# Optimization experiments

Hardware: AMD Instinct MI355X
Metric: run time of the kernel (lower is better)

The kernel has to match this reference:

```python
import jax, jax.numpy as jnp
import numpy as np

N0 = 100000; E0 = 1600000; N1 = 100000; E1 = 1600000; G = 512
F0 = 93; F1 = 43
BN_EPS = 1e-5


def setup_inputs() -> dict:
    key = jax.random.key(0)
    ks = jax.random.split(key, 20)
    p = lambda i, shape: jax.random.normal(ks[i], shape, jnp.float32) * 0.02
    return {
        "x_0": jax.random.normal(ks[0], (N0, F0), jnp.float32),
        "x_1": jax.random.normal(ks[1], (N1, F1), jnp.float32),
        "edge_index_0": jax.random.randint(ks[2], (2, E0), 0, N0, jnp.int32),
        "edge_index_1": jax.random.randint(ks[3], (2, E1), 0, N1, jnp.int32),
        "batch_0": jnp.sort(jax.random.randint(ks[4], (N0,), 0, G, jnp.int32)),
        "batch_1": jnp.sort(jax.random.randint(ks[5], (N1,), 0, G, jnp.int32)),
        "w_c1": p(6, (F0, F0)), "b_c1": jnp.zeros((F0,), jnp.float32),
        "w_c2": p(7, (F0, F0 * 10)), "b_c2": jnp.zeros((F0 * 10,), jnp.float32),
        "w_c3": p(8, (F1, F1)), "b_c3": jnp.zeros((F1,), jnp.float32),
        "w_c4": p(9, (F1, F1 * 10)), "b_c4": jnp.zeros((F1 * 10,), jnp.float32),
        "g0_w1": p(10, (F0 * 10 * 2, 1024)), "g0_b1": jnp.zeros((1024,), jnp.float32),
        "g0_w2": p(11, (1024, 512)), "g0_b2": jnp.zeros((512,), jnp.float32),
        "g0_bn_g": jnp.ones((512,), jnp.float32), "g0_bn_b": jnp.zeros((512,), jnp.float32),
        "g1_w1": p(12, (F1 * 10 * 2, 1024)), "g1_b1": jnp.zeros((1024,), jnp.float32),
        "g1_w2": p(13, (1024, 512)), "g1_b2": jnp.zeros((512,), jnp.float32),
        "g1_bn_g": jnp.ones((512,), jnp.float32), "g1_bn_b": jnp.zeros((512,), jnp.float32),
        "f0_w1": p(14, (512, 256)), "f0_b1": jnp.zeros((256,), jnp.float32),
        "f0_w2": p(15, (256, 2)), "f0_b2": jnp.zeros((2,), jnp.float32),
        "f1_w1": p(16, (512, 256)), "f1_b1": jnp.zeros((256,), jnp.float32),
        "f1_w2": p(17, (256, 2)), "f1_b2": jnp.zeros((2,), jnp.float32),
    }


def gin_conv(x, edge_index, W, b):
    # GINConv(eps=0): nn(x + sum_{j->i} x_j); messages from src=edge_index[0] to dst=edge_index[1]
    agg = jax.ops.segment_sum(x[edge_index[0]], edge_index[1], num_segments=x.shape[0])
    return (x + agg) @ W + b


def pool_mean_max(x, batch):
    cnt = jax.ops.segment_sum(jnp.ones((x.shape[0], 1), x.dtype), batch, num_segments=G)
    mean = jax.ops.segment_sum(x, batch, num_segments=G) / jnp.maximum(cnt, 1.0)
    mx = jax.ops.segment_max(x, batch, num_segments=G)
    mx = jnp.where(cnt > 0, mx, 0.0)
    return jnp.concatenate([mean, mx], axis=1)


def batchnorm(x, g, b):
    m = x.mean(axis=0)
    v = x.var(axis=0)
    return g * (x - m) / jnp.sqrt(v + BN_EPS) + b


def branch(x, ei, batch, w_a, b_a, w_b, b_b, w1, b1, w2, b2, bn_g, bn_b):
    h = jax.nn.relu(gin_conv(x, ei, w_a, b_a))
    h = jax.nn.relu(gin_conv(h, ei, w_b, b_b))
    h = pool_mean_max(h, batch)              # [G, 2*10*F] ; PairNorm(mode='None') is identity
    h = jax.nn.relu(h @ w1 + b1)             # dropout: eval mode (identity)
    h = h @ w2 + b2
    return batchnorm(h, bn_g, bn_b)          # [G, 512]


def reference(x_0, x_1, edge_index_0, edge_index_1, batch_0, batch_1,
              w_c1, b_c1, w_c2, b_c2, w_c3, b_c3, w_c4, b_c4,
              g0_w1, g0_b1, g0_w2, g0_b2, g0_bn_g, g0_bn_b,
              g1_w1, g1_b1, g1_w2, g1_b2, g1_bn_g, g1_bn_b,
              f0_w1, f0_b1, f0_w2, f0_b2, f1_w1, f1_b1, f1_w2, f1_b2):
    x_g_0 = branch(x_0, edge_index_0, batch_0, w_c1, b_c1, w_c2, b_c2,
                   g0_w1, g0_b1, g0_w2, g0_b2, g0_bn_g, g0_bn_b)
    z = jax.nn.relu(x_g_0 @ f0_w1 + f0_b1) @ f0_w2 + f0_b2
    x_g_1 = branch(x_1, edge_index_1, batch_1, w_c3, b_c3, w_c4, b_c4,
                   g1_w1, g1_b1, g1_w2, g1_b2, g1_bn_g, g1_bn_b)
    z1 = jax.nn.relu(x_g_1 @ f1_w1 + f1_b1) @ f1_w2 + f1_b2
    return (z, x_g_0, x_g_1, z1)
```

## Files before the change

### kernel.cpp

```cpp
#include <hip/hip_runtime.h>
#include <hip/hip_bf16.h>

#define N0 100000
#define E0C 1600000
#define N1 100000
#define E1C 1600000
#define GCONST 512
#define F0C 93
#define F1C 43
#define OC0 (F0C * 10)
#define OC1 (F1C * 10)
#define BN_EPS 1e-5f
#define NBKT 391
#define SLAB 6016

typedef __attribute__((ext_vector_type(8))) short short8;
typedef __attribute__((ext_vector_type(4))) float floatx4;

static __device__ __forceinline__ unsigned short f2bf(float f) {
    unsigned u = __float_as_uint(f);
    unsigned r = (u + 0x7FFF + ((u >> 16) & 1)) >> 16;
    return (unsigned short)r;
}
static __device__ __forceinline__ float bf2f(unsigned short u) {
    return __uint_as_float(((unsigned)u) << 16);
}
static __device__ __forceinline__ void split_bf(float v, unsigned short& h, unsigned short& l) {
    h = f2bf(v);
    l = f2bf(v - bf2f(h));
}

__global__ __launch_bounds__(256) void misc_kernel(const int* __restrict__ bat0,
                                                   const int* __restrict__ bat1,
                                                   int* __restrict__ st0,
                                                   int* __restrict__ st1,
                                                   int* __restrict__ bcur2,
                                                   float* __restrict__ bnsum0,
                                                   float* __restrict__ bnsum1) {
    int bid = blockIdx.x;
    int t = threadIdx.x;
    if (bid < 6) {
        int branch = bid / 3;
        const int* batch = branch ? bat1 : bat0;
        int* starts = branch ? st1 : st0;
        int g = (bid % 3) * 256 + t;
        if (g > GCONST) return;
        if (g == GCONST) { starts[GCONST] = N0; return; }
        int lo = 0, hi = N0;
        while (lo < hi) {
            int mid = (lo + hi) >> 1;
            if (batch[mid] < g) lo = mid + 1; else hi = mid;
        }
        starts[g] = lo;
    } else if (bid == 6) {
        for (int i = t; i < 1024; i += 256) {
            if (i < NBKT) bcur2[i] = i * SLAB;
            else if (i >= 512 && i < 512 + NBKT) bcur2[i] = (i - 512) * SLAB;
        }
    } else {
        for (int i = t; i < 1024; i += 256) {
            bnsum0[i] = 0.f;
            bnsum1[i] = 0.f;
        }
    }
}

__global__ __launch_bounds__(256) void edge_bucket2_kernel(const int* __restrict__ ei0,
                                                           const int* __restrict__ ei1,
                                                           int E, int* __restrict__ bcur2,
                                                           int2* __restrict__ st0,
                                                           int2* __restrict__ st1,
                                                           const float* __restrict__ Wc1,
                                                           const float* __restrict__ Wc2,
                                                           const float* __restrict__ Wc3,
                                                           const float* __restrict__ Wc4,
                                                           unsigned short* __restrict__ Ta0,
                                                           unsigned short* __restrict__ Tb0,
                                                           unsigned short* __restrict__ Ta1,
                                                           unsigned short* __restrict__ Tb1,
                                                           unsigned short* __restrict__ p0h,
                                                           unsigned short* __restrict__ p0l,
                                                           unsigned short* __restrict__ p1h,
                                                           unsigned short* __restrict__ p1l) {
    int bid = blockIdx.x;
    int t = threadIdx.x;
    if (bid < 1564) {
        int branch = bid >= 782;
        int blk = branch ? bid - 782 : bid;
        const int* ei = branch ? ei1 : ei0;
        int* bcur = bcur2 + branch * 512;
        int2* staging = branch ? st1 : st0;
        __shared__ int hist[NBKT];
        __shared__ int gbase[NBKT];
        for (int i = t; i < NBKT; i += 256) hist[i] = 0;
        __syncthreads();
        int base = blk * 2048;
        int srcv[8], dstv[8];
#pragma unroll
        for (int i = 0; i < 8; ++i) {
            int e = base + i * 256 + t;
            if (e < E) { srcv[i] = ei[e]; dstv[i] = ei[E + e]; }
            else dstv[i] = -1;
        }
#pragma unroll
        for (int i = 0; i < 8; ++i)
            if (dstv[i] >= 0) atomicAdd(&hist[dstv[i] >> 8], 1);
        __syncthreads();
        for (int i = t; i < NBKT; i += 256) {
            int c = hist[i];
            gbase[i] = c ? atomicAdd(&bcur[i], c) : 0;
            hist[i] = 0;
        }
        __syncthreads();
#pragma unroll
        for (int i = 0; i < 8; ++i) {
            if (dstv[i] >= 0) {
                int b = dstv[i] >> 8;
                int lofs = atomicAdd(&hist[b], 1);
                staging[gbase[b] + lofs] = make_int2(srcv[i], dstv[i]);
            }
        }
    } else if (bid < 3612) {
        int idx = bid - 1564;
        int cfg = idx >> 9;
        int c = (idx & 511) * 2 + (t >> 7);
        int k = t & 127;
        const float* W; unsigned short* T; int OCr, Fr, KP, RB;
        switch (cfg) {
            case 0:  W = Wc1; T = Ta0; OCr = 93;  Fr = 93; KP = 96; RB = 96;   break;
            case 1:  W = Wc2; T = Tb0; OCr = 930; Fr = 93; KP = 96; RB = 1024; break;
            case 2:  W = Wc3; T = Ta1; OCr = 43;  Fr = 43; KP = 64; RB = 48;   break;
            default: W = Wc4; T = Tb1; OCr = 430; Fr = 43; KP = 64; RB = 512;  break;
        }
        if (c >= RB || k >= KP) return;
        unsigned short v = 0;
        if (c < OCr && k < Fr) v = f2bf(W[(size_t)k * OCr + c]);
        T[(size_t)c * KP + k] = v;
    } else if (bid < 3732) {
        int i = (bid - 3612) * 256 + t;
        if (i >= GCONST * 60) return;
        int g = i / 60, c = 1860 + (i - g * 60);
        p0h[(size_t)g * 1920 + c] = 0;
        p0l[(size_t)g * 1920 + c] = 0;
    } else {
        int i = (bid - 3732) * 256 + t;
        if (i >= GCONST * 36) return;
        int g = i / 36, c = 860 + (i - g * 36);
        p1h[(size_t)g * 896 + c] = 0;
        p1l[(size_t)g * 896 + c] = 0;
    }
}

__global__ __launch_bounds__(512) void bucket_scan2_kernel(const int* __restrict__ bcur2,
                                                           int* __restrict__ bbase2) {
    const int* bcur = bcur2 + blockIdx.x * 512;
    int* bbase = bbase2 + blockIdx.x * 512;
    __shared__ int sh[512];
    int t = threadIdx.x;
    int cnt = (t < NBKT) ? bcur[t] - t * SLAB : 0;
    sh[t] = cnt;
    __syncthreads();
    for (int o = 1; o < 512; o <<= 1) {
        int add = (t >= o) ? sh[t - o] : 0;
        __syncthreads();
        sh[t] += add;
        __syncthreads();
    }
    if (t <= NBKT) bbase[t] = sh[t] - cnt;
}

static __device__ __forceinline__ void csr_build_dev(int b, const int2* __restrict__ staging,
                                                     const int* __restrict__ bcur,
                                                     const int* __restrict__ bbase, int N,
                                                     int* __restrict__ rowptr,
                                                     int* __restrict__ col) {
    __shared__ int h[256];
    __shared__ int sc[256];
    int t = threadIdx.x;
    int sl = b * SLAB;
    int se = bcur[b];
    int go = bbase[b];
    h[t] = 0;
    __syncthreads();
    for (int i = sl + t; i < se; i += 256)
        atomicAdd(&h[staging[i].y & 255], 1);
    __syncthreads();
    int v = h[t];
    sc[t] = v;
    __syncthreads();
    for (int o = 1; o < 256; o <<= 1) {
        int add = (t >= o) ? sc[t - o] : 0;
        __syncthreads();
        sc[t] += add;
        __syncthreads();
    }
    int ex = go + (sc[t] - v);
    int node = (b << 8) + t;
    if (node <= N) rowptr[node] = ex;
    __syncthreads();
    sc[t] = ex;
    __syncthreads();
    for (int i = sl + t; i < se; i += 256) {
        int2 ed = staging[i];
        int pos = atomicAdd(&sc[ed.y & 255], 1);
        col[pos] = ed.x;
    }
}

static __device__ __forceinline__ void wsplit_dev(int k0, int c0,
                                                  const float* __restrict__ W,
                                                  unsigned short* __restrict__ Th,
                                                  unsigned short* __restrict__ Tl,
                                                  int K, int N, int KP) {
    __shared__ float tile[32][33];
    int tx = threadIdx.x & 31, ty = threadIdx.x >> 5;
    for (int r = ty; r < 32; r += 8) {
        int k = k0 + r;
        tile[r][tx] = (k < K) ? W[(size_t)k * N + c0 + tx] : 0.f;
    }
    __syncthreads();
    for (int r = ty; r < 32; r += 8) {
        int c = c0 + r;
        float v = tile[tx][r];
        unsigned short h, l;
        split_bf(v, h, l);
        Th[(size_t)c * KP + k0 + tx] = h;
        Tl[(size_t)c * KP + k0 + tx] = l;
    }
}

template<int KP, int CH, int GR>
static __device__ __forceinline__ void gather_dev(int nb, unsigned short* __restrict__ t,
                                                  const unsigned short* __restrict__ x,
                                                  const int* __restrict__ rowptr,
                                                  const int* __restrict__ col, int N) {
    int wave = threadIdx.x >> 6, lane = threadIdx.x & 63;
    int node = nb * 4 + wave;
    if (node >= N) return;
    int g = lane / CH;
    int c = lane - g * CH;
    bool act = (g < GR);
    int s = rowptr[node], e = rowptr[node + 1];
    float acc[8] = {0.f, 0.f, 0.f, 0.f, 0.f, 0.f, 0.f, 0.f};
    int j = act ? (s - 1 + g) : e;
    int src0 = node;
    if (j >= s && j < e) src0 = col[j];
    while (j < e) {
        int jb = j + GR;
        int jc = jb + GR;
        int srcb = (jb < e) ? col[jb] : 0;
        int srcc = (jc < e) ? col[jc] : 0;
        short8 v0 = *(const short8*)(x + (size_t)src0 * KP + c * 8);
#pragma unroll
        for (int i = 0; i < 8; ++i) acc[i] += bf2f((unsigned short)v0[i]);
        if (jb < e) {
            short8 v1 = *(const short8*)(x + (size_t)srcb * KP + c * 8);
#pragma unroll
            for (int i = 0; i < 8; ++i) acc[i] += bf2f((unsigned short)v1[i]);
        }
        j = jc; src0 = srcc;
    }
    if (GR == 8) {
#pragma unroll
        for (int i = 0; i < 8; ++i) {
            float v = acc[i];
            v += __shfl_xor(v, 8);
            v += __shfl_xor(v, 16);
            v += __shfl_xor(v, 32);
            acc[i] = v;
        }
    } else {
#pragma unroll
        for (int i = 0; i < 8; ++i) {
            float v = acc[i];
            float v1 = __shfl(v, lane + CH);
            float v2 = __shfl(v, lane + 2 * CH);
            float v3 = __shfl(v, lane + 3 * CH);
            float v4 = __shfl(v, lane + 4 * CH);
            acc[i] = v + v1 + v2 + v3 + v4;
        }
    }
    if (lane < CH) {
        short8 o;
#pragma unroll
        for (int i = 0; i < 8; ++i) o[i] = (short)f2bf(acc[i]);
        *(short8*)(t + (size_t)node * KP + lane * 8) = o;
    }
}

template<int KP, int KS, int NT>
static __device__ __forceinline__ void conv1_dev(int nb, const unsigned short* __restrict__ t,
                                                 const unsigned short* __restrict__ Wt,
                                                 const float* __restrict__ bias,
                                                 unsigned short* __restrict__ y,
                                                 int NC, int N) {
    int wave = threadIdx.x >> 6, lane = threadIdx.x & 63;
    int quad = lane >> 4, l15 = lane & 15;
    int r0 = (nb * 4 + wave) * 16;
    const short8 z8 = {0, 0, 0, 0, 0, 0, 0, 0};
    short8 a[KS];
    int arow = r0 + l15;
#pragma unroll
    for (int ks = 0; ks < KS; ++ks)
        a[ks] = (arow < N) ? *(const short8*)(t + (size_t)arow * KP + ks * 32 + quad * 8) : z8;
#pragma unroll
    for (int nt = 0; nt < NT; ++nt) {
        int colb = nt * 16 + l15;
        floatx4 c = {0.f, 0.f, 0.f, 0.f};
#pragma unroll
        for (int ks = 0; ks < KS; ++ks) {
            short8 b = *(const short8*)(Wt + (size_t)colb * KP + ks * 32 + quad * 8);
            c = __builtin_amdgcn_mfma_f32_16x16x32_bf16(a[ks], b, c, 0, 0, 0);
        }
        float bc = (colb < NC) ? bias[colb] : 0.f;
#pragma unroll
        for (int r = 0; r < 4; ++r) {
            int row = r0 + quad * 4 + r;
            if (row < N) {
                float o = fmaxf(c[r] + bc, 0.f);
                y[(size_t)row * KP + colb] = f2bf(o);
            }
        }
    }
}

template<int KP, int KS>
static __device__ __forceinline__ void conv2_pool_dev(int cb, int g,
                                                      const unsigned short* __restrict__ t,
                                                      const unsigned short* __restrict__ Wt,
                                                      const float* __restrict__ bias,
                                                      const int* __restrict__ starts,
                                                      unsigned short* __restrict__ ph,
                                                      unsigned short* __restrict__ pl,
                                                      int OC, int KPad) {
    int wave = threadIdx.x >> 6, lane = threadIdx.x & 63;
    int quad = lane >> 4, l15 = lane & 15;
    int cw0 = cb * 256 + wave * 64;
    short8 bfr[4][KS];
    float bs[4];
#pragma unroll
    for (int ti = 0; ti < 4; ++ti) {
        int colb = cw0 + ti * 16 + l15;
#pragma unroll
        for (int ks = 0; ks < KS; ++ks)
            bfr[ti][ks] = *(const short8*)(Wt + (size_t)colb * KP + ks * 32 + quad * 8);
        bs[ti] = (colb < OC) ? bias[colb] : 0.f;
    }
    int s = starts[g], e = starts[g + 1];
    float sum[4] = {0.f, 0.f, 0.f, 0.f};
    float mx[4]  = {0.f, 0.f, 0.f, 0.f};
    const short8 z8 = {0, 0, 0, 0, 0, 0, 0, 0};
    for (int ns = s; ns < e; ns += 16) {
        short8 a[KS];
        int arow = ns + l15;
        bool av = arow < e;
#pragma unroll
        for (int ks = 0; ks < KS; ++ks)
            a[ks] = av ? *(const short8*)(t + (size_t)arow * KP + ks * 32 + quad * 8) : z8;
        int rbase = ns + quad * 4;
#pragma unroll
        for (int ti = 0; ti < 4; ++ti) {
            floatx4 c = {0.f, 0.f, 0.f, 0.f};
#pragma unroll
            for (int ks = 0; ks < KS; ++ks)
                c = __builtin_amdgcn_mfma_f32_16x16x32_bf16(a[ks], bfr[ti][ks], c, 0, 0, 0);
#pragma unroll
            for (int r = 0; r < 4; ++r) {
                float o = fmaxf(c[r] + bs[ti], 0.f);
                if (rbase + r < e) {
                    sum[ti] += o;
                    mx[ti] = fmaxf(mx[ti], o);
                }
            }
        }
    }
    int cnt = e - s;
    float rc = 1.f / (float)(cnt > 0 ? cnt : 1);
#pragma unroll
    for (int ti = 0; ti < 4; ++ti) {
        float sv = sum[ti], mv = mx[ti];
        sv += __shfl_down(sv, 32);
        mv = fmaxf(mv, __shfl_down(mv, 32));
        sv += __shfl_down(sv, 16);
        mv = fmaxf(mv, __shfl_down(mv, 16));
        if (lane < 16) {
            int colb = cw0 + ti * 16 + l15;
            if (colb < OC) {
                size_t base = (size_t)g * (size_t)KPad;
                unsigned short h, l;
                split_bf(sv * rc, h, l);
                ph[base + colb] = h; pl[base + colb] = l;
                split_bf(mv, h, l);
                ph[base + OC + colb] = h; pl[base + OC + colb] = l;
            }
        }
    }
}

template<int MODE>
static __device__ __forceinline__ void gemm3x_dev(int bx, int by, int NBX,
                                                  const unsigned short* __restrict__ Ah,
                                                  const unsigned short* __restrict__ Al,
                                                  const unsigned short* __restrict__ Bh,
                                                  const unsigned short* __restrict__ Bl,
                                                  const float* __restrict__ bias,
                                                  float* __restrict__ Cf,
                                                  unsigned short* __restrict__ Ch,
                                                  unsigned short* __restrict__ Cl,
                                                  int KP,
                                                  float* __restrict__ bnsum = nullptr) {
    int wave = threadIdx.x >> 6, lane = threadIdx.x & 63;
    int quad = lane >> 4, l15 = lane & 15;
    int r0 = by * 32 + (wave & 1) * 16;
    int c0 = bx * 64 + (wave >> 1) * 32;
    int Ncols = NBX * 64;
    floatx4 acc0 = {0.f, 0.f, 0.f, 0.f};
    floatx4 acc1 = {0.f, 0.f, 0.f, 0.f};
    const unsigned short* arh = Ah + (size_t)(r0 + l15) * KP;
    const unsigned short* arl = Al + (size_t)(r0 + l15) * KP;
    const unsigned short* b0h = Bh + (size_t)(c0 + l15) * KP;
    const unsigned short* b0l = Bl + (size_t)(c0 + l15) * KP;
    const unsigned short* b1h = Bh + (size_t)(c0 + 16 + l15) * KP;
    const unsigned short* b1l = Bl + (size_t)(c0 + 16 + l15) * KP;
    for (int k0 = 0; k0 < KP; k0 += 128) {
        short8 ah[4], al[4];
#pragma unroll
        for (int q = 0; q < 4; ++q) {
            ah[q] = *(const short8*)(arh + k0 + q * 32 + quad * 8);
            al[q] = *(const short8*)(arl + k0 + q * 32 + quad * 8);
        }
#pragma unroll
        for (int q = 0; q < 4; ++q) {
            short8 bh = *(const short8*)(b0h + k0 + q * 32 + quad * 8);
            short8 bl = *(const short8*)(b0l + k0 + q * 32 + quad * 8);
            acc0 = __builtin_amdgcn_mfma_f32_16x16x32_bf16(ah[q], bh, acc0, 0, 0, 0);
            acc0 = __builtin_amdgcn_mfma_f32_16x16x32_bf16(al[q], bh, acc0, 0, 0, 0);
            acc0 = __builtin_amdgcn_mfma_f32_16x16x32_bf16(ah[q], bl, acc0, 0, 0, 0);
            bh = *(const short8*)(b1h + k0 + q * 32 + quad * 8);
            bl = *(const short8*)(b1l + k0 + q * 32 + quad * 8);
            acc1 = __builtin_amdgcn_mfma_f32_16x16x32_bf16(ah[q], bh, acc1, 0, 0, 0);
            acc1 = __builtin_amdgcn_mfma_f32_16x16x32_bf16(al[q], bh, acc1, 0, 0, 0);
            acc1 = __builtin_amdgcn_mfma_f32_16x16x32_bf16(ah[q], bl, acc1, 0, 0, 0);
        }
    }
    int col0 = c0 + l15, col1 = c0 + 16 + l15;
    float bc0 = bias[col0], bc1 = bias[col1];
    if (MODE == 3) {
        __shared__ float lsum[64], lsum2[64];
        if (threadIdx.x < 64) { lsum[threadIdx.x] = 0.f; lsum2[threadIdx.x] = 0.f; }
        __syncthreads();
        float p0 = 0.f, p0q = 0.f, p1 = 0.f, p1q = 0.f;
#pragma unroll
        for (int r = 0; r < 4; ++r) {
            int row = r0 + quad * 4 + r;
            float v0 = acc0[r] + bc0;
            float v1 = acc1[r] + bc1;
            Cf[(size_t)row * Ncols + col0] = v0;
            Cf[(size_t)row * Ncols + col1] = v1;
            p0 += v0; p0q += v0 * v0;
            p1 += v1; p1q += v1 * v1;
        }
        int cl0 = (wave >> 1) * 32 + l15;
        atomicAdd(&lsum[cl0], p0);       atomicAdd(&lsum2[cl0], p0q);
        atomicAdd(&lsum[cl0 + 16], p1);  atomicAdd(&lsum2[cl0 + 16], p1q);
        __syncthreads();
        if (threadIdx.x < 64) {
            atomicAdd(&bnsum[bx * 64 + threadIdx.x], lsum[threadIdx.x]);
            atomicAdd(&bnsum[512 + bx * 64 + threadIdx.x], lsum2[threadIdx.x]);
        }
        return;
    }
#pragma unroll
    for (int r = 0; r < 4; ++r) {
        int row = r0 + quad * 4 + r;
        float v0 = acc0[r] + bc0;
        float v1 = acc1[r] + bc1;
        if (MODE == 0 || MODE == 2) { v0 = fmaxf(v0, 0.f); v1 = fmaxf(v1, 0.f); }
        if (MODE == 0) {
            unsigned short h, l;
            split_bf(v0, h, l);
            Ch[(size_t)row * Ncols + col0] = h; Cl[(size_t)row * Ncols + col0] = l;
            split_bf(v1, h, l);
            Ch[(size_t)row * Ncols + col1] = h; Cl[(size_t)row * Ncols + col1] = l;
        } else {
            Cf[(size_t)row * Ncols + col0] = v0;
            Cf[(size_t)row * Ncols + col1] = v1;
        }
    }
}

static __device__ __forceinline__ void head2_dev(int nb, const float* __restrict__ h,
                                                 const float* __restrict__ w2,
                                                 const float* __restrict__ b2,
                                                 float* __restrict__ z, int M) {
    int wave = threadIdx.x >> 6, lane = threadIdx.x & 63;
    int row = nb * 4 + wave;
    if (row >= M) return;
    float4 hv = *(const float4*)(h + (size_t)row * 256 + lane * 4);
    const float* wp = w2 + lane * 8;
    float s0 = hv.x * wp[0] + hv.y * wp[2] + hv.z * wp[4] + hv.w * wp[6];
    float s1 = hv.x * wp[1] + hv.y * wp[3] + hv.z * wp[5] + hv.w * wp[7];
#pragma unroll
    for (int offd = 32; offd >= 1; offd >>= 1) {
        s0 += __shfl_down(s0, offd);
        s1 += __shfl_down(s1, offd);
    }
    if (lane == 0) {
        z[(size_t)row * 2 + 0] = s0 + b2[0];
        z[(size_t)row * 2 + 1] = s1 + b2[1];
    }
}


__global__ __launch_bounds__(256) void f0_kernel(const int2* __restrict__ st0,
                                                 const int2* __restrict__ st1,
                                                 const int* __restrict__ bcur2,
                                                 const int* __restrict__ bbase2,
                                                 int* __restrict__ rp0, int* __restrict__ rp1,
                                                 int* __restrict__ c0, int* __restrict__ c1,
                                                 unsigned short* __restrict__ xb0,
                                                 const float* __restrict__ x0,
                                                 unsigned short* __restrict__ xb1,
                                                 const float* __restrict__ x1) {
    int bid = blockIdx.x;
    if (bid < 2 * NBKT) {
        int branch = bid >= NBKT;
        csr_build_dev(branch ? bid - NBKT : bid,
                      branch ? st1 : st0,
                      bcur2 + branch * 512, bbase2 + branch * 512, N0,
                      branch ? rp1 : rp0, branch ? c1 : c0);
    } else if (bid < 2 * NBKT + 50000) {
        int b = bid - 2 * NBKT;
        int node = b * 2 + (threadIdx.x >> 7);
        int f = threadIdx.x & 127;
        if (node < N0 && f < 96)
            xb0[(size_t)node * 96 + f] = (f < 93) ? f2bf(x0[(size_t)node * 93 + f]) : (unsigned short)0;
    } else {
        int b = bid - 2 * NBKT - 50000;
        int node = b * 4 + (threadIdx.x >> 6);
        int f = threadIdx.x & 63;
        if (node < N1)
            xb1[(size_t)node * 64 + f] = (f < 43) ? f2bf(x1[(size_t)node * 43 + f]) : (unsigned short)0;
    }
}

__global__ __launch_bounds__(256) void f1_kernel(unsigned short* __restrict__ tb,
                                                 const unsigned short* __restrict__ xb0,
                                                 const int* __restrict__ rowptr0,
                                                 const int* __restrict__ col0,
                                                 const float* g0_w1, const float* g0_w2,
                                                 const float* f0_w1,
                                                 const float* g1_w1, const float* g1_w2,
                                                 const float* f1_w1,
                                                 unsigned short* bt1h0, unsigned short* bt1l0,
                                                 unsigned short* bt2h0, unsigned short* bt2l0,
                                                 unsigned short* bt3h0, unsigned short* bt3l0,
                                                 unsigned short* bt1h1, unsigned short* bt1l1,
                                                 unsigned short* bt2h1, unsigned short* bt2l1,
                                                 unsigned short* bt3h1, unsigned short* bt3l1) {
    int bid = blockIdx.x;
    if (bid < 25000) {
        gather_dev<96, 12, 5>(bid, tb, xb0, rowptr0, col0, N0);
        return;
    }
    int w = bid - 25000;
    if (w < 1920)      wsplit_dev((w % 60) * 32, (w / 60) * 32, g0_w1, bt1h0, bt1l0, 1860, 1024, 1920);
    else if (w < 2432) { w -= 1920; wsplit_dev((w % 32) * 32, (w / 32) * 32, g0_w2, bt2h0, bt2l0, 1024, 512, 1024); }
    else if (w < 2560) { w -= 2432; wsplit_dev((w % 16) * 32, (w / 16) * 32, f0_w1, bt3h0, bt3l0, 512, 256, 512); }
    else if (w < 3456) { w -= 2560; wsplit_dev((w % 28) * 32, (w / 28) * 32, g1_w1, bt1h1, bt1l1, 860, 1024, 896); }
    else if (w < 3968) { w -= 3456; wsplit_dev((w % 32) * 32, (w / 32) * 32, g1_w2, bt2h1, bt2l1, 1024, 512, 1024); }
    else               { w -= 3968; wsplit_dev((w % 16) * 32, (w / 16) * 32, f1_w1, bt3h1, bt3l1, 512, 256, 512); }
}

__global__ __launch_bounds__(256) void f2_kernel(unsigned short* __restrict__ t1,
                                                 const unsigned short* __restrict__ xb1,
                                                 const int* __restrict__ rowptr1,
                                                 const int* __restrict__ col1,
                                                 const unsigned short* __restrict__ tb,
                                                 const unsigned short* __restrict__ wt_a0,
                                                 const float* __restrict__ b_c1,
                                                 unsigned short* __restrict__ yb) {
    int bid = blockIdx.x;
    if (bid < 25000)
        gather_dev<64, 8, 8>(bid, t1, xb1, rowptr1, col1, N1);
    else
        conv1_dev<96, 3, 6>(bid - 25000, tb, wt_a0, b_c1, yb, 93, N0);
}

__global__ __launch_bounds__(256) void f3_kernel(unsigned short* __restrict__ tb,
                                                 const unsigned short* __restrict__ yb,
                                                 const int* __restrict__ rowptr0,
                                                 const int* __restrict__ col0,
                                                 const unsigned short* __restrict__ t1,
                                                 const unsigned short* __restrict__ wt_a1,
                                                 const float* __restrict__ b_c3,
                                                 unsigned short* __restrict__ y1) {
    int bid = blockIdx.x;
    if (bid < 25000)
        gather_dev<96, 12, 5>(bid, tb, yb, rowptr0, col0, N0);
    else
        conv1_dev<64, 2, 3>(bid - 25000, t1, wt_a1, b_c3, y1, 43, N1);
}

__global__ __launch_bounds__(256) void f4_kernel(unsigned short* __restrict__ t1,
                                                 const unsigned short* __restrict__ y1,
                                                 const int* __restrict__ rowptr1,
                                                 const int* __restrict__ col1) {
    gather_dev<64, 8, 8>(blockIdx.x, t1, y1, rowptr1, col1, N1);
}

__global__ __launch_bounds__(256) void f5_kernel(const unsigned short* __restrict__ tb,
                                                 const unsigned short* __restrict__ wt_b0,
                                                 const float* __restrict__ b_c2,
                                                 const int* __restrict__ starts0,
                                                 unsigned short* __restrict__ p0h,
                                                 unsigned short* __restrict__ p0l,
                                                 const unsigned short* __restrict__ t1,
                                                 const unsigned short* __restrict__ wt_b1,
                                                 const float* __restrict__ b_c4,
                                                 const int* __restrict__ starts1,
                                                 unsigned short* __restrict__ p1h,
                                                 unsigned short* __restrict__ p1l) {
    int bid = blockIdx.x;
    if (bid < 2048) {
        int b = bid;
        int g = (b & 7) | ((b >> 5) << 3);
        int cb = (b >> 3) & 3;
        conv2_pool_dev<96, 3>(cb, g, tb, wt_b0, b_c2, starts0, p0h, p0l, OC0, 1920);
    } else {
        int b = bid - 2048;
        int g = (b & 7) | ((b >> 4) << 3);
        int cb = (b >> 3) & 1;
        conv2_pool_dev<64, 2>(cb, g, t1, wt_b1, b_c4, starts1, p1h, p1l, OC1, 896);
    }
}

__global__ __launch_bounds__(256) void f6_kernel(const unsigned short* __restrict__ p0h,
                                                 const unsigned short* __restrict__ p0l,
                                                 const unsigned short* __restrict__ bt1h0,
                                                 const unsigned short* __restrict__ bt1l0,
                                                 const float* __restrict__ g0_b1,
                                                 unsigned short* __restrict__ m1h0,
                                                 unsigned short* __restrict__ m1l0,
                                                 const unsigned short* __restrict__ p1h,
                                                 const unsigned short* __restrict__ p1l,
                                                 const unsigned short* __restrict__ bt1h1,
                                                 const unsigned short* __restrict__ bt1l1,
                                                 const float* __restrict__ g1_b1,
                                                 unsigned short* __restrict__ m1h1,
                                                 unsigned short* __restrict__ m1l1) {
    int bid = blockIdx.x;
    if (bid < 256)
        gemm3x_dev<0>(bid & 15, bid >> 4, 16, p0h, p0l, bt1h0, bt1l0, g0_b1,
                      nullptr, m1h0, m1l0, 1920);
    else {
        int b = bid - 256;
        gemm3x_dev<0>(b & 15, b >> 4, 16, p1h, p1l, bt1h1, bt1l1, g1_b1,
                      nullptr, m1h1, m1l1, 896);
    }
}

__global__ __launch_bounds__(256) void f7_kernel(const unsigned short* __restrict__ m1h0,
                                                 const unsigned short* __restrict__ m1l0,
                                                 const unsigned short* __restrict__ bt2h0,
                                                 const unsigned short* __restrict__ bt2l0,
                                                 const float* __restrict__ g0_b2,
                                                 float* __restrict__ pbn0,
                                                 float* __restrict__ bnsum0,
                                                 const unsigned short* __restrict__ m1h1,
                                                 const unsigned short* __restrict__ m1l1,
                                                 const unsigned short* __restrict__ bt2h1,
                                                 const unsigned short* __restrict__ bt2l1,
                                                 const float* __restrict__ g1_b2,
                                                 float* __restrict__ pbn1,
                                                 float* __restrict__ bnsum1) {
    int bid = blockIdx.x;
    if (bid < 128)
        gemm3x_dev<3>(bid & 7, bid >> 3, 8, m1h0, m1l0, bt2h0, bt2l0, g0_b2,
                      pbn0, nullptr, nullptr, 1024, bnsum0);
    else {
        int b = bid - 128;
        gemm3x_dev<3>(b & 7, b >> 3, 8, m1h1, m1l1, bt2h1, bt2l1, g1_b2,
                      pbn1, nullptr, nullptr, 1024, bnsum1);
    }
}

__global__ __launch_bounds__(256) void f8_kernel(const float* __restrict__ pbn0,
                                                 const float* __restrict__ bnsum0,
                                                 const float* __restrict__ g0_bn_g,
                                                 const float* __restrict__ g0_bn_b,
                                                 float* __restrict__ out_xg0,
                                                 unsigned short* __restrict__ xgh0,
                                                 unsigned short* __restrict__ xgl0,
                                                 const float* __restrict__ pbn1,
                                                 const float* __restrict__ bnsum1,
                                                 const float* __restrict__ g1_bn_g,
                                                 const float* __restrict__ g1_bn_b,
                                                 float* __restrict__ out_xg1,
                                                 unsigned short* __restrict__ xgh1,
                                                 unsigned short* __restrict__ xgl1) {
    int bid = blockIdx.x;
    int branch = bid >= 512;
    int row = branch ? bid - 512 : bid;
    const float* p   = branch ? pbn1 : pbn0;
    const float* bs  = branch ? bnsum1 : bnsum0;
    const float* gam = branch ? g1_bn_g : g0_bn_g;
    const float* bet = branch ? g1_bn_b : g0_bn_b;
    float* outp = branch ? out_xg1 : out_xg0;
    unsigned short* oh = branch ? xgh1 : xgh0;
    unsigned short* ol = branch ? xgl1 : xgl0;
    int t = threadIdx.x;
#pragma unroll
    for (int k = 0; k < 2; ++k) {
        int c = t + k * 256;
        float s = bs[c], s2 = bs[512 + c];
        float m = s * (1.f / 512.f);
        float var = s2 * (1.f / 512.f) - m * m;
        float iv = 1.f / sqrtf(var + BN_EPS);
        float x = p[(size_t)row * 512 + c];
        float v = gam[c] * (x - m) * iv + bet[c];
        outp[(size_t)row * 512 + c] = v;
        unsigned short h, l;
        split_bf(v, h, l);
        oh[(size_t)row * 512 + c] = h;
        ol[(size_t)row * 512 + c] = l;
    }
}

__global__ __launch_bounds__(256) void f9_kernel(const unsigned short* __restrict__ xgh0,
                                                 const unsigned short* __restrict__ xgl0,
                                                 const unsigned short* __restrict__ bt3h0,
                                                 const unsigned short* __restrict__ bt3l0,
                                                 const float* __restrict__ f0_b1,
                                                 float* __restrict__ hbuf0,
                                                 const unsigned short* __restrict__ xgh1,
                                                 const unsigned short* __restrict__ xgl1,
                                                 const unsigned short* __restrict__ bt3h1,
                                                 const unsigned short* __restrict__ bt3l1,
                                                 const float* __restrict__ f1_b1,
                                                 float* __restrict__ hbuf1) {
    int bid = blockIdx.x;
    if (bid < 64)
        gemm3x_dev<2>(bid & 3, bid >> 2, 4, xgh0, xgl0, bt3h0, bt3l0, f0_b1,
                      hbuf0, nullptr, nullptr, 512);
    else {
        int b = bid - 64;
        gemm3x_dev<2>(b & 3, b >> 2, 4, xgh1, xgl1, bt3h1, bt3l1, f1_b1,
                      hbuf1, nullptr, nullptr, 512);
    }
}

__global__ __launch_bounds__(256) void f10_kernel(const float* __restrict__ hbuf0,
                                                  const float* __restrict__ f0_w2,
                                                  const float* __restrict__ f0_b2,
                                                  float* __restrict__ out_z,
                                                  const float* __restrict__ hbuf1,
                                                  const float* __restrict__ f1_w2,
                                                  const float* __restrict__ f1_b2,
                                                  float* __restrict__ out_z1) {
    int bid = blockIdx.x;
    if (bid < 128)
        head2_dev(bid, hbuf0, f0_w2, f0_b2, out_z, GCONST);
    else
        head2_dev(bid - 128, hbuf1, f1_w2, f1_b2, out_z1, GCONST);
}

static inline int ceildiv(int a, int b) { return (a + b - 1) / b; }

extern "C" void kernel_launch(void* const* d_in, const int* in_sizes, int n_in,
                              void* d_out, int out_size, void* d_ws, size_t ws_size,
                              hipStream_t stream) {
    const float* x0   = (const float*)d_in[0];
    const float* x1   = (const float*)d_in[1];
    const int*   ei0  = (const int*)d_in[2];
    const int*   ei1  = (const int*)d_in[3];
    const int*   bat0 = (const int*)d_in[4];
    const int*   bat1 = (const int*)d_in[5];
    const float* w_c1 = (const float*)d_in[6];
    const float* b_c1 = (const float*)d_in[7];
    const float* w_c2 = (const float*)d_in[8];
    const float* b_c2 = (const float*)d_in[9];
    const float* w_c3 = (const float*)d_in[10];
    const float* b_c3 = (const float*)d_in[11];
    const float* w_c4 = (const float*)d_in[12];
    const float* b_c4 = (const float*)d_in[13];
    const float* g0_w1 = (const float*)d_in[14];
    const float* g0_b1 = (const float*)d_in[15];
    const float* g0_w2 = (const float*)d_in[16];
    const float* g0_b2 = (const float*)d_in[17];
    const float* g0_bn_g = (const float*)d_in[18];
    const float* g0_bn_b = (const float*)d_in[19];
    const float* g1_w1 = (const float*)d_in[20];
    const float* g1_b1 = (const float*)d_in[21];
    const float* g1_w2 = (const float*)d_in[22];
    const float* g1_b2 = (const float*)d_in[23];
    const float* g1_bn_g = (const float*)d_in[24];
    const float* g1_bn_b = (const float*)d_in[25];
    const float* f0_w1 = (const float*)d_in[26];
    const float* f0_b1 = (const float*)d_in[27];
    const float* f0_w2 = (const float*)d_in[28];
    const float* f0_b2 = (const float*)d_in[29];
    const float* f1_w1 = (const float*)d_in[30];
    const float* f1_b1 = (const float*)d_in[31];
    const float* f1_w2 = (const float*)d_in[32];
    const float* f1_b2 = (const float*)d_in[33];

    float* out = (float*)d_out;
    float* out_z   = out;
    float* out_xg0 = out + 1024;
    float* out_xg1 = out + 1024 + 262144;
    float* out_z1  = out + 1024 + 262144 + 262144;

    float* ws = (float*)d_ws;
    size_t off = 0;
    auto alloc = [&](size_t n) { float* p = ws + off; off += n; return p; };
    unsigned short* xb0 = (unsigned short*)alloc((size_t)N0 * 96 / 2);
    unsigned short* xb1 = (unsigned short*)alloc((size_t)N1 * 64 / 2);
    unsigned short* tb  = (unsigned short*)alloc((size_t)N0 * 96 / 2);
    unsigned short* yb  = (unsigned short*)alloc((size_t)N0 * 96 / 2);
    unsigned short* wt_a0 = (unsigned short*)alloc(96 * 96 / 2);
    unsigned short* wt_b0 = (unsigned short*)alloc(1024 * 96 / 2);
    unsigned short* wt_a1 = (unsigned short*)alloc(48 * 64 / 2);
    unsigned short* wt_b1 = (unsigned short*)alloc(512 * 64 / 2);
    unsigned short* bt1h0 = (unsigned short*)alloc((size_t)1024 * 1920 / 2);
    unsigned short* bt1l0 = (unsigned short*)alloc((size_t)1024 * 1920 / 2);
    unsigned short* bt2h0 = (unsigned short*)alloc((size_t)512 * 1024 / 2);
    unsigned short* bt2l0 = (unsigned short*)alloc((size_t)512 * 1024 / 2);
    unsigned short* bt3h0 = (unsigned short*)alloc((size_t)256 * 512 / 2);
    unsigned short* bt3l0 = (unsigned short*)alloc((size_t)256 * 512 / 2);
    unsigned short* bt1h1 = (unsigned short*)alloc((size_t)1024 * 896 / 2);
    unsigned short* bt1l1 = (unsigned short*)alloc((size_t)1024 * 896 / 2);
    unsigned short* bt2h1 = (unsigned short*)alloc((size_t)512 * 1024 / 2);
    unsigned short* bt2l1 = (unsigned short*)alloc((size_t)512 * 1024 / 2);
    unsigned short* bt3h1 = (unsigned short*)alloc((size_t)256 * 512 / 2);
    unsigned short* bt3l1 = (unsigned short*)alloc((size_t)256 * 512 / 2);
    unsigned short* m1h0 = (unsigned short*)alloc((size_t)512 * 1024 / 2);
    unsigned short* m1l0 = (unsigned short*)alloc((size_t)512 * 1024 / 2);
    unsigned short* m1h1 = (unsigned short*)alloc((size_t)512 * 1024 / 2);
    unsigned short* m1l1 = (unsigned short*)alloc((size_t)512 * 1024 / 2);
    unsigned short* xgh0 = (unsigned short*)alloc((size_t)512 * 512 / 2);
    unsigned short* xgl0 = (unsigned short*)alloc((size_t)512 * 512 / 2);
    unsigned short* xgh1 = (unsigned short*)alloc((size_t)512 * 512 / 2);
    unsigned short* xgl1 = (unsigned short*)alloc((size_t)512 * 512 / 2);
    unsigned short* p0h = (unsigned short*)alloc((size_t)512 * 1920 / 2);
    unsigned short* p0l = (unsigned short*)alloc((size_t)512 * 1920 / 2);
    unsigned short* p1h = (unsigned short*)alloc((size_t)512 * 896 / 2);
    unsigned short* p1l = (unsigned short*)alloc((size_t)512 * 896 / 2);
    float* pbn0  = alloc((size_t)512 * 512);
    float* pbn1  = alloc((size_t)512 * 512);
    float* hbuf0 = alloc((size_t)512 * 256);
    float* hbuf1 = alloc((size_t)512 * 256);
    float* bnsum0 = alloc(1024);
    float* bnsum1 = alloc(1024);
    int* bbase2 = (int*)alloc(1024);
    int* bcur2  = (int*)alloc(1024);
    int* rowptr0 = (int*)alloc(100016);
    int* col0    = (int*)alloc(E0C);
    int* rowptr1 = (int*)alloc(100016);
    int* col1    = (int*)alloc(E1C);
    int* starts0 = (int*)alloc(520);
    int* starts1 = (int*)alloc(520);
    int2* staging0 = (int2*)tb;
    int2* staging1 = (int2*)yb;
    unsigned short* t1 = xb0;
    unsigned short* y1 = xb1;

    misc_kernel<<<8, 256, 0, stream>>>(bat0, bat1, starts0, starts1, bcur2,
                                       bnsum0, bnsum1);
    edge_bucket2_kernel<<<3804, 256, 0, stream>>>(ei0, ei1, E0C, bcur2,
                                                  staging0, staging1,
                                                  w_c1, w_c2, w_c3, w_c4,
                                                  wt_a0, wt_b0, wt_a1, wt_b1,
                                                  p0h, p0l, p1h, p1l);
    bucket_scan2_kernel<<<2, 512, 0, stream>>>(bcur2, bbase2);
    f0_kernel<<<2 * NBKT + 50000 + 25000, 256, 0, stream>>>(
        staging0, staging1, bcur2, bbase2, rowptr0, rowptr1, col0, col1,
        xb0, x0, xb1, x1);

    f1_kernel<<<25000 + 4096, 256, 0, stream>>>(
        tb, xb0, rowptr0, col0,
        g0_w1, g0_w2, f0_w1, g1_w1, g1_w2, f1_w1,
        bt1h0, bt1l0, bt2h0, bt2l0, bt3h0, bt3l0,
        bt1h1, bt1l1, bt2h1, bt2l1, bt3h1, bt3l1);
    f2_kernel<<<25000 + 1563, 256, 0, stream>>>(t1, xb1, rowptr1, col1,
                                                tb, wt_a0, b_c1, yb);
    f3_kernel<<<25000 + 1563, 256, 0, stream>>>(tb, yb, rowptr0, col0,
                                                t1, wt_a1, b_c3, y1);
    f4_kernel<<<25000, 256, 0, stream>>>(t1, y1, rowptr1, col1);
    f5_kernel<<<2048 + 1024, 256, 0, stream>>>(tb, wt_b0, b_c2, starts0, p0h, p0l,
                                               t1, wt_b1, b_c4, starts1, p1h, p1l);
    f6_kernel<<<256 + 256, 256, 0, stream>>>(p0h, p0l, bt1h0, bt1l0, g0_b1, m1h0, m1l0,
                                             p1h, p1l, bt1h1, bt1l1, g1_b1, m1h1, m1l1);
    f7_kernel<<<128 + 128, 256, 0, stream>>>(m1h0, m1l0, bt2h0, bt2l0, g0_b2, pbn0, bnsum0,
                                             m1h1, m1l1, bt2h1, bt2l1, g1_b2, pbn1, bnsum1);
    f8_kernel<<<512 + 512, 256, 0, stream>>>(pbn0, bnsum0, g0_bn_g, g0_bn_b, out_xg0, xgh0, xgl0,
                                             pbn1, bnsum1, g1_bn_g, g1_bn_b, out_xg1, xgh1, xgl1);
    f9_kernel<<<64 + 64, 256, 0, stream>>>(xgh0, xgl0, bt3h0, bt3l0, f0_b1, hbuf0,
                                           xgh1, xgl1, bt3h1, bt3l1, f1_b1, hbuf1);
    f10_kernel<<<128 + 128, 256, 0, stream>>>(hbuf0, f0_w2, f0_b2, out_z,
                                              hbuf1, f1_w2, f1_b2, out_z1);
}
```

Measured before the change: 654.4 us.

## Merge bucketing, x conversion, and weight splits into one prologue; drop scan kernel

Moves the x-to-bf16 conversion and the MLP weight hi/lo splits into the edge bucketing kernel, making one large prologue launch. The separate bucket scan kernel goes away: each CSR-build block now sums the counts of the earlier buckets itself with a block reduction. This cuts two launches and the serialization between them, and the gather kernel no longer runs the weight-split tail. In exchange each CSR block does redundant prefix work (up to 391 reads plus a reduction), and the prologue's long grid tail may delay CSR construction.

```diff
diff --git a/kernel.cpp b/kernel.cpp
--- a/kernel.cpp
+++ b/kernel.cpp
@@ -65,23 +65,59 @@
     }
 }
 
-__global__ __launch_bounds__(256) void edge_bucket2_kernel(const int* __restrict__ ei0,
-                                                           const int* __restrict__ ei1,
-                                                           int E, int* __restrict__ bcur2,
-                                                           int2* __restrict__ st0,
-                                                           int2* __restrict__ st1,
-                                                           const float* __restrict__ Wc1,
-                                                           const float* __restrict__ Wc2,
-                                                           const float* __restrict__ Wc3,
-                                                           const float* __restrict__ Wc4,
-                                                           unsigned short* __restrict__ Ta0,
-                                                           unsigned short* __restrict__ Tb0,
-                                                           unsigned short* __restrict__ Ta1,
-                                                           unsigned short* __restrict__ Tb1,
-                                                           unsigned short* __restrict__ p0h,
-                                                           unsigned short* __restrict__ p0l,
-                                                           unsigned short* __restrict__ p1h,
-                                                           unsigned short* __restrict__ p1l) {
+static __device__ __forceinline__ void wsplit_dev(int k0, int c0,
+                                                  const float* __restrict__ W,
+                                                  unsigned short* __restrict__ Th,
+                                                  unsigned short* __restrict__ Tl,
+                                                  int K, int N, int KP) {
+    __shared__ float tile[32][33];
+    int tx = threadIdx.x & 31, ty = threadIdx.x >> 5;
+    for (int r = ty; r < 32; r += 8) {
+        int k = k0 + r;
+        tile[r][tx] = (k < K) ? W[(size_t)k * N + c0 + tx] : 0.f;
+    }
+    __syncthreads();
+    for (int r = ty; r < 32; r += 8) {
+        int c = c0 + r;
+        float v = tile[tx][r];
+        unsigned short h, l;
+        split_bf(v, h, l);
+        Th[(size_t)c * KP + k0 + tx] = h;
+        Tl[(size_t)c * KP + k0 + tx] = l;
+    }
+}
+
+__global__ __launch_bounds__(256) void prologue_kernel(const int* __restrict__ ei0,
+                                                       const int* __restrict__ ei1,
+                                                       int E, int* __restrict__ bcur2,
+                                                       int2* __restrict__ st0,
+                                                       int2* __restrict__ st1,
+                                                       const float* __restrict__ Wc1,
+                                                       const float* __restrict__ Wc2,
+                                                       const float* __restrict__ Wc3,
+                                                       const float* __restrict__ Wc4,
+                                                       unsigned short* __restrict__ Ta0,
+                                                       unsigned short* __restrict__ Tb0,
+                                                       unsigned short* __restrict__ Ta1,
+                                                       unsigned short* __restrict__ Tb1,
+                                                       unsigned short* __restrict__ p0h,
+                                                       unsigned short* __restrict__ p0l,
+                                                       unsigned short* __restrict__ p1h,
+                                                       unsigned short* __restrict__ p1l,
+                                                       const float* __restrict__ x0,
+                                                       unsigned short* __restrict__ xb0,
+                                                       const float* __restrict__ x1,
+                                                       unsigned short* __restrict__ xb1,
+                                                       const float* g0_w1, const float* g0_w2,
+                                                       const float* f0_w1,
+                                                       const float* g1_w1, const float* g1_w2,
+                                                       const float* f1_w1,
+                                                       unsigned short* bt1h0, unsigned short* bt1l0,
+                                                       unsigned short* bt2h0, unsigned short* bt2l0,
+                                                       unsigned short* bt3h0, unsigned short* bt3l0,
+                                                       unsigned short* bt1h1, unsigned short* bt1l1,
+                                                       unsigned short* bt2h1, unsigned short* bt2l1,
+                                                       unsigned short* bt3h1, unsigned short* bt3l1) {
     int bid = blockIdx.x;
     int t = threadIdx.x;
     if (bid < 1564) {
@@ -142,44 +178,56 @@
         int g = i / 60, c = 1860 + (i - g * 60);
         p0h[(size_t)g * 1920 + c] = 0;
         p0l[(size_t)g * 1920 + c] = 0;
-    } else {
+    } else if (bid < 3804) {
         int i = (bid - 3732) * 256 + t;
         if (i >= GCONST * 36) return;
         int g = i / 36, c = 860 + (i - g * 36);
         p1h[(size_t)g * 896 + c] = 0;
         p1l[(size_t)g * 896 + c] = 0;
-    }
-}
-
-__global__ __launch_bounds__(512) void bucket_scan2_kernel(const int* __restrict__ bcur2,
-                                                           int* __restrict__ bbase2) {
-    const int* bcur = bcur2 + blockIdx.x * 512;
-    int* bbase = bbase2 + blockIdx.x * 512;
-    __shared__ int sh[512];
-    int t = threadIdx.x;
-    int cnt = (t < NBKT) ? bcur[t] - t * SLAB : 0;
-    sh[t] = cnt;
-    __syncthreads();
-    for (int o = 1; o < 512; o <<= 1) {
-        int add = (t >= o) ? sh[t - o] : 0;
-        __syncthreads();
-        sh[t] += add;
-        __syncthreads();
-    }
-    if (t <= NBKT) bbase[t] = sh[t] - cnt;
+    } else if (bid < 7900) {
+        int w = bid - 3804;
+        if (w < 1920)      wsplit_dev((w % 60) * 32, (w / 60) * 32, g0_w1, bt1h0, bt1l0, 1860, 1024, 1920);
+        else if (w < 2432) { w -= 1920; wsplit_dev((w % 32) * 32, (w / 32) * 32, g0_w2, bt2h0, bt2l0, 1024, 512, 1024); }
+        else if (w < 2560) { w -= 2432; wsplit_dev((w % 16) * 32, (w / 16) * 32, f0_w1, bt3h0, bt3l0, 512, 256, 512); }
+        else if (w < 3456) { w -= 2560; wsplit_dev((w % 28) * 32, (w / 28) * 32, g1_w1, bt1h1, bt1l1, 860, 1024, 896); }
+        else if (w < 3968) { w -= 3456; wsplit_dev((w % 32) * 32, (w / 32) * 32, g1_w2, bt2h1, bt2l1, 1024, 512, 1024); }
+        else               { w -= 3968; wsplit_dev((w % 16) * 32, (w / 16) * 32, f1_w1, bt3h1, bt3l1, 512, 256, 512); }
+    } else if (bid < 57900) {
+        int b = bid - 7900;
+        int node = b * 2 + (t >> 7);
+        int f = t & 127;
+        if (node < N0 && f < 96)
+            xb0[(size_t)node * 96 + f] = (f < 93) ? f2bf(x0[(size_t)node * 93 + f]) : (unsigned short)0;
+    } else {
+        int b = bid - 57900;
+        int node = b * 4 + (t >> 6);
+        int f = t & 63;
+        if (node < N1)
+            xb1[(size_t)node * 64 + f] = (f < 43) ? f2bf(x1[(size_t)node * 43 + f]) : (unsigned short)0;
+    }
 }
 
 static __device__ __forceinline__ void csr_build_dev(int b, const int2* __restrict__ staging,
-                                                     const int* __restrict__ bcur,
-                                                     const int* __restrict__ bbase, int N,
+                                                     const int* __restrict__ bcur, int N,
                                                      int* __restrict__ rowptr,
                                                      int* __restrict__ col) {
     __shared__ int h[256];
     __shared__ int sc[256];
+    __shared__ int goS;
     int t = threadIdx.x;
+    int acc = 0;
+    for (int i = t; i < b; i += 256) acc += bcur[i] - i * SLAB;
+    h[t] = acc;
+    __syncthreads();
+    for (int st = 128; st > 0; st >>= 1) {
+        if (t < st) h[t] += h[t + st];
+        __syncthreads();
+    }
+    if (t == 0) goS = h[0];
+    __syncthreads();
+    int go = goS;
     int sl = b * SLAB;
     int se = bcur[b];
-    int go = bbase[b];
     h[t] = 0;
     __syncthreads();
     for (int i = sl + t; i < se; i += 256)
@@ -204,28 +252,6 @@
         int2 ed = staging[i];
         int pos = atomicAdd(&sc[ed.y & 255], 1);
         col[pos] = ed.x;
-    }
-}
-
-static __device__ __forceinline__ void wsplit_dev(int k0, int c0,
-                                                  const float* __restrict__ W,
-                                                  unsigned short* __restrict__ Th,
-                                                  unsigned short* __restrict__ Tl,
-                                                  int K, int N, int KP) {
-    __shared__ float tile[32][33];
-    int tx = threadIdx.x & 31, ty = threadIdx.x >> 5;
-    for (int r = ty; r < 32; r += 8) {
-        int k = k0 + r;
-        tile[r][tx] = (k < K) ? W[(size_t)k * N + c0 + tx] : 0.f;
-    }
-    __syncthreads();
-    for (int r = ty; r < 32; r += 8) {
-        int c = c0 + r;
-        float v = tile[tx][r];
-        unsigned short h, l;
-        split_bf(v, h, l);
-        Th[(size_t)c * KP + k0 + tx] = h;
-        Tl[(size_t)c * KP + k0 + tx] = l;
     }
 }
 
@@ -515,61 +541,21 @@
 __global__ __launch_bounds__(256) void f0_kernel(const int2* __restrict__ st0,
                                                  const int2* __restrict__ st1,
                                                  const int* __restrict__ bcur2,
-                                                 const int* __restrict__ bbase2,
                                                  int* __restrict__ rp0, int* __restrict__ rp1,
-                                                 int* __restrict__ c0, int* __restrict__ c1,
-                                                 unsigned short* __restrict__ xb0,
-                                                 const float* __restrict__ x0,
-                                                 unsigned short* __restrict__ xb1,
-                                                 const float* __restrict__ x1) {
-    int bid = blockIdx.x;
-    if (bid < 2 * NBKT) {
-        int branch = bid >= NBKT;
-        csr_build_dev(branch ? bid - NBKT : bid,
-                      branch ? st1 : st0,
-                      bcur2 + branch * 512, bbase2 + branch * 512, N0,
-                      branch ? rp1 : rp0, branch ? c1 : c0);
-    } else if (bid < 2 * NBKT + 50000) {
-        int b = bid - 2 * NBKT;
-        int node = b * 2 + (threadIdx.x >> 7);
-        int f = threadIdx.x & 127;
-        if (node < N0 && f < 96)
-            xb0[(size_t)node * 96 + f] = (f < 93) ? f2bf(x0[(size_t)node * 93 + f]) : (unsigned short)0;
-    } else {
-        int b = bid - 2 * NBKT - 50000;
-        int node = b * 4 + (threadIdx.x >> 6);
-        int f = threadIdx.x & 63;
-        if (node < N1)
-            xb1[(size_t)node * 64 + f] = (f < 43) ? f2bf(x1[(size_t)node * 43 + f]) : (unsigned short)0;
-    }
+                                                 int* __restrict__ c0, int* __restrict__ c1) {
+    int bid = blockIdx.x;
+    int branch = bid >= NBKT;
+    csr_build_dev(branch ? bid - NBKT : bid,
+                  branch ? st1 : st0,
+                  bcur2 + branch * 512, N0,
+                  branch ? rp1 : rp0, branch ? c1 : c0);
 }
 
 __global__ __launch_bounds__(256) void f1_kernel(unsigned short* __restrict__ tb,
                                                  const unsigned short* __restrict__ xb0,
                                                  const int* __restrict__ rowptr0,
-                                                 const int* __restrict__ col0,
-                                                 const float* g0_w1, const float* g0_w2,
-                                                 const float* f0_w1,
-                                                 const float* g1_w1, const float* g1_w2,
-                                                 const float* f1_w1,
-                                                 unsigned short* bt1h0, unsigned short* bt1l0,
-                                                 unsigned short* bt2h0, unsigned short* bt2l0,
-                                                 unsigned short* bt3h0, unsigned short* bt3l0,
-                                                 unsigned short* bt1h1, unsigned short* bt1l1,
-                                                 unsigned short* bt2h1, unsigned short* bt2l1,
-                                                 unsigned short* bt3h1, unsigned short* bt3l1) {
-    int bid = blockIdx.x;
-    if (bid < 25000) {
-        gather_dev<96, 12, 5>(bid, tb, xb0, rowptr0, col0, N0);
-        return;
-    }
-    int w = bid - 25000;
-    if (w < 1920)      wsplit_dev((w % 60) * 32, (w / 60) * 32, g0_w1, bt1h0, bt1l0, 1860, 1024, 1920);
-    else if (w < 2432) { w -= 1920; wsplit_dev((w % 32) * 32, (w / 32) * 32, g0_w2, bt2h0, bt2l0, 1024, 512, 1024); }
-    else if (w < 2560) { w -= 2432; wsplit_dev((w % 16) * 32, (w / 16) * 32, f0_w1, bt3h0, bt3l0, 512, 256, 512); }
-    else if (w < 3456) { w -= 2560; wsplit_dev((w % 28) * 32, (w / 28) * 32, g1_w1, bt1h1, bt1l1, 860, 1024, 896); }
-    else if (w < 3968) { w -= 3456; wsplit_dev((w % 32) * 32, (w / 32) * 32, g1_w2, bt2h1, bt2l1, 1024, 512, 1024); }
-    else               { w -= 3968; wsplit_dev((w % 16) * 32, (w / 16) * 32, f1_w1, bt3h1, bt3l1, 512, 256, 512); }
+                                                 const int* __restrict__ col0) {
+    gather_dev<96, 12, 5>(blockIdx.x, tb, xb0, rowptr0, col0, N0);
 }
 
 __global__ __launch_bounds__(256) void f2_kernel(unsigned short* __restrict__ t1,
@@ -852,7 +838,6 @@
     float* hbuf1 = alloc((size_t)512 * 256);
     float* bnsum0 = alloc(1024);
     float* bnsum1 = alloc(1024);
-    int* bbase2 = (int*)alloc(1024);
     int* bcur2  = (int*)alloc(1024);
     int* rowptr0 = (int*)alloc(100016);
     int* col0    = (int*)alloc(E0C);
@@ -867,21 +852,18 @@
 
     misc_kernel<<<8, 256, 0, stream>>>(bat0, bat1, starts0, starts1, bcur2,
                                        bnsum0, bnsum1);
-    edge_bucket2_kernel<<<3804, 256, 0, stream>>>(ei0, ei1, E0C, bcur2,
-                                                  staging0, staging1,
-                                                  w_c1, w_c2, w_c3, w_c4,
-                                                  wt_a0, wt_b0, wt_a1, wt_b1,
-                                                  p0h, p0l, p1h, p1l);
-    bucket_scan2_kernel<<<2, 512, 0, stream>>>(bcur2, bbase2);
-    f0_kernel<<<2 * NBKT + 50000 + 25000, 256, 0, stream>>>(
-        staging0, staging1, bcur2, bbase2, rowptr0, rowptr1, col0, col1,
-        xb0, x0, xb1, x1);
-
-    f1_kernel<<<25000 + 4096, 256, 0, stream>>>(
-        tb, xb0, rowptr0, col0,
+    prologue_kernel<<<82900, 256, 0, stream>>>(
+        ei0, ei1, E0C, bcur2, staging0, staging1,
+        w_c1, w_c2, w_c3, w_c4, wt_a0, wt_b0, wt_a1, wt_b1,
+        p0h, p0l, p1h, p1l,
+        x0, xb0, x1, xb1,
         g0_w1, g0_w2, f0_w1, g1_w1, g1_w2, f1_w1,
         bt1h0, bt1l0, bt2h0, bt2l0, bt3h0, bt3l0,
         bt1h1, bt1l1, bt2h1, bt2l1, bt3h1, bt3l1);
+    f0_kernel<<<2 * NBKT, 256, 0, stream>>>(staging0, staging1, bcur2,
+                                            rowptr0, rowptr1, col0, col1);
+
+    f1_kernel<<<25000, 256, 0, stream>>>(tb, xb0, rowptr0, col0);
     f2_kernel<<<25000 + 1563, 256, 0, stream>>>(t1, xb1, rowptr1, col1,
                                                 tb, wt_a0, b_c1, yb);
     f3_kernel<<<25000 + 1563, 256, 0, stream>>>(tb, yb, rowptr0, col0,
```

Result: no change. 657.7 us (+0.5%).
